# Kernel optimization log

Measured on AMD Instinct MI355X. Metric: run time of the kernel, lower is better.

Reference implementation:

```python
import jax, jax.numpy as jnp
import numpy as np

B, N, D = 32, 50000, 64  # batch, node_num, num_inputs


def setup_inputs() -> dict:
    key = jax.random.key(0)
    k1, k2, k3 = jax.random.split(key, 3)
    x = jax.random.normal(k1, (B, N, D), dtype=jnp.float32)
    # xavier_uniform_ with gain=1.414 on a (2D, 1) matrix: bound = gain*sqrt(6/(fan_in+fan_out))
    bound = 1.414 * np.sqrt(6.0 / (2 * D + 1))
    a = jax.random.uniform(k2, (2 * D, 1), minval=-bound, maxval=bound, dtype=jnp.float32)
    adj_mask = jax.random.randint(k3, (N,), 0, 2).astype(jnp.int32)
    node_index = 123  # scalar target-node index
    return {"x": x, "a": a, "node_index": node_index, "adj_mask": adj_mask}


def reference(x, a, node_index, adj_mask):
    # torch: concat([x[:, idx].expand(node_num), x], -1) @ a  ==  x[:, idx] @ a[:D] + x @ a[D:]
    d = x.shape[-1]
    a_tgt = a[:d, 0]   # weights applied to the (broadcast) target-node features
    a_src = a[d:, 0]   # weights applied to every node's own features
    tgt_score = x[:, node_index] @ a_tgt          # [B]
    e = jax.nn.leaky_relu(tgt_score[:, None] + x @ a_src, negative_slope=0.01)  # [B, N]
    neg = jnp.asarray(-9e15, e.dtype)
    masked = jnp.where(adj_mask > 0, e, neg)
    attention = jax.nn.softmax(masked, axis=1) * adj_mask.astype(e.dtype)[None, :]
    return attention
```

## Files before the change

### kernel.cpp

```cpp
#include <hip/hip_runtime.h>

#define NN 50000
#define DD 64
#define BB 32
#define TILE 256

__global__ __launch_bounds__(256) void attn_pass1(
    const float* __restrict__ x, const float* __restrict__ a,
    const int* __restrict__ node_index, const int* __restrict__ adj,
    float* __restrict__ out, float* __restrict__ sums)
{
    const int tid = threadIdx.x;
    const int b = blockIdx.y;
    const int rowBase = blockIdx.x * TILE;
    const int node = *node_index;

    __shared__ int   sh_adj[TILE];
    __shared__ float sh_p[TILE];
    __shared__ float sh_tgt;
    __shared__ float sh_part[4];

    {
        const int r = rowBase + tid;
        sh_adj[tid] = (r < NN) ? adj[r] : 0;
    }

    if (tid < 64) {
        float v = x[(size_t)b * NN * DD + (size_t)node * DD + tid] * a[tid];
        #pragma unroll
        for (int o = 32; o >= 1; o >>= 1) v += __shfl_xor(v, o, 64);
        if (tid == 0) sh_tgt = v;
    }
    __syncthreads();
    const float tgt = sh_tgt;

    const int wave = tid >> 6;
    const int lane = tid & 63;
    const int g = lane >> 4;
    const int c = lane & 15;

    const float4 av = ((const float4*)(a + DD))[c];
    const float* xb = x + (size_t)b * NN * DD;

    float local = 0.f;

    #pragma unroll
    for (int h = 0; h < 2; h++) {
        int   msk[8];
        float4 xv[8];
        #pragma unroll
        for (int u = 0; u < 8; u++) {
            const int lrow = wave * 64 + h * 32 + u * 4 + g;
            msk[u] = sh_adj[lrow];
            if (msk[u] > 0) {
                const size_t row = (size_t)(rowBase + lrow);
                xv[u] = ((const float4*)(xb + row * DD))[c];
            } else {
                xv[u] = make_float4(0.f, 0.f, 0.f, 0.f);
            }
        }
        #pragma unroll
        for (int u = 0; u < 8; u++) {
            float s = xv[u].x * av.x + xv[u].y * av.y + xv[u].z * av.z + xv[u].w * av.w;
            s += __shfl_xor(s, 1, 64);
            s += __shfl_xor(s, 2, 64);
            s += __shfl_xor(s, 4, 64);
            s += __shfl_xor(s, 8, 64);
            if (c == 0) {
                const int lrow = wave * 64 + h * 32 + u * 4 + g;
                float p = 0.f;
                if (msk[u] > 0) {
                    const float z = tgt + s;
                    const float e = (z > 0.f) ? z : 0.01f * z;
                    p = __expf(e);
                }
                sh_p[lrow] = p;
                local += p;
            }
        }
    }

    #pragma unroll
    for (int o = 32; o >= 1; o >>= 1) local += __shfl_xor(local, o, 64);
    if (lane == 0) sh_part[wave] = local;
    __syncthreads();
    if (tid == 0)
        atomicAdd(&sums[b], sh_part[0] + sh_part[1] + sh_part[2] + sh_part[3]);

    {
        const int r = rowBase + tid;
        if (r < NN) out[(size_t)b * NN + r] = sh_p[tid];
    }
}

__global__ __launch_bounds__(256) void attn_pass2(
    float* __restrict__ out, const float* __restrict__ sums)
{
    const int N4 = NN / 4;
    const int f = blockIdx.x * blockDim.x + threadIdx.x;
    const int b = blockIdx.y;
    if (f < N4) {
        const float inv = 1.0f / sums[b];
        float4* p = (float4*)out + (size_t)b * N4 + f;
        float4 v = *p;
        v.x *= inv; v.y *= inv; v.z *= inv; v.w *= inv;
        *p = v;
    }
}

extern "C" void kernel_launch(void* const* d_in, const int* in_sizes, int n_in,
                              void* d_out, int out_size, void* d_ws, size_t ws_size,
                              hipStream_t stream) {
    const float* x = (const float*)d_in[0];
    const float* a = (const float*)d_in[1];
    const int* node_index = (const int*)d_in[2];
    const int* adj = (const int*)d_in[3];
    float* out = (float*)d_out;
    float* sums = (float*)d_ws;

    hipMemsetAsync(sums, 0, BB * sizeof(float), stream);

    dim3 g1((NN + TILE - 1) / TILE, BB);
    attn_pass1<<<g1, 256, 0, stream>>>(x, a, node_index, adj, out, sums);

    dim3 g2((NN / 4 + 255) / 256, BB);
    attn_pass2<<<g2, 256, 0, stream>>>(out, sums);
}
```

Before: 506.8 us.

## Use 4 lanes per row with strided float4 loads and drop atomics/memset

Pass 1 now assigns 4 lanes per row. Each lane loads four float4 chunks strided across the row, which needs only two shuffle steps instead of four. The per-block partial sums are written to a workspace array instead of being combined with atomicAdd, and pass 2 reduces the 196 partials per batch itself. This removes the memset launch and atomic contention, at the cost of each pass-2 block redundantly re-reducing the partials. The load pattern changes from one contiguous 256B row segment per 16 lanes to interleaved 64B pieces, which could affect coalescing.

```diff
diff --git a/kernel.cpp b/kernel.cpp
--- a/kernel.cpp
+++ b/kernel.cpp
@@ -4,11 +4,12 @@
 #define DD 64
 #define BB 32
 #define TILE 256
+#define NPB ((NN + TILE - 1) / TILE)
 
 __global__ __launch_bounds__(256) void attn_pass1(
     const float* __restrict__ x, const float* __restrict__ a,
     const int* __restrict__ node_index, const int* __restrict__ adj,
-    float* __restrict__ out, float* __restrict__ sums)
+    float* __restrict__ out, float* __restrict__ pbs )
 {
     const int tid = threadIdx.x;
     const int b = blockIdx.y;
@@ -36,47 +37,45 @@
 
     const int wave = tid >> 6;
     const int lane = tid & 63;
-    const int g = lane >> 4;
-    const int c = lane & 15;
+    const int c  = lane & 3;
+    const int rg = lane >> 2;
 
-    const float4 av = ((const float4*)(a + DD))[c];
+    const float4* a4 = (const float4*)(a + DD);
+    const float4 av0 = a4[c + 0];
+    const float4 av1 = a4[c + 4];
+    const float4 av2 = a4[c + 8];
+    const float4 av3 = a4[c + 12];
+
     const float* xb = x + (size_t)b * NN * DD;
-
     float local = 0.f;
 
     #pragma unroll
-    for (int h = 0; h < 2; h++) {
-        int   msk[8];
-        float4 xv[8];
-        #pragma unroll
-        for (int u = 0; u < 8; u++) {
-            const int lrow = wave * 64 + h * 32 + u * 4 + g;
-            msk[u] = sh_adj[lrow];
-            if (msk[u] > 0) {
-                const size_t row = (size_t)(rowBase + lrow);
-                xv[u] = ((const float4*)(xb + row * DD))[c];
-            } else {
-                xv[u] = make_float4(0.f, 0.f, 0.f, 0.f);
+    for (int i = 0; i < 4; i++) {
+        const int lrow = wave * 64 + i * 16 + rg;
+        const int msk = sh_adj[lrow];
+        float s = 0.f;
+        if (msk > 0) {
+            const float4* xr = (const float4*)(xb + (size_t)(rowBase + lrow) * DD);
+            const float4 v0 = xr[c + 0];
+            const float4 v1 = xr[c + 4];
+            const float4 v2 = xr[c + 8];
+            const float4 v3 = xr[c + 12];
+            s  = v0.x * av0.x + v0.y * av0.y + v0.z * av0.z + v0.w * av0.w;
+            s += v1.x * av1.x + v1.y * av1.y + v1.z * av1.z + v1.w * av1.w;
+            s += v2.x * av2.x + v2.y * av2.y + v2.z * av2.z + v2.w * av2.w;
+            s += v3.x * av3.x + v3.y * av3.y + v3.z * av3.z + v3.w * av3.w;
+        }
+        s += __shfl_xor(s, 1, 64);
+        s += __shfl_xor(s, 2, 64);
+        if (c == 0) {
+            float p = 0.f;
+            if (msk > 0) {
+                const float z = tgt + s;
+                const float e = (z > 0.f) ? z : 0.01f * z;
+                p = __expf(e);
             }
-        }
-        #pragma unroll
-        for (int u = 0; u < 8; u++) {
-            float s = xv[u].x * av.x + xv[u].y * av.y + xv[u].z * av.z + xv[u].w * av.w;
-            s += __shfl_xor(s, 1, 64);
-            s += __shfl_xor(s, 2, 64);
-            s += __shfl_xor(s, 4, 64);
-            s += __shfl_xor(s, 8, 64);
-            if (c == 0) {
-                const int lrow = wave * 64 + h * 32 + u * 4 + g;
-                float p = 0.f;
-                if (msk[u] > 0) {
-                    const float z = tgt + s;
-                    const float e = (z > 0.f) ? z : 0.01f * z;
-                    p = __expf(e);
-                }
-                sh_p[lrow] = p;
-                local += p;
-            }
+            sh_p[lrow] = p;
+            local += p;
         }
     }
 
@@ -85,7 +84,7 @@
     if (lane == 0) sh_part[wave] = local;
     __syncthreads();
     if (tid == 0)
-        atomicAdd(&sums[b], sh_part[0] + sh_part[1] + sh_part[2] + sh_part[3]);
+        pbs[b * NPB + blockIdx.x] = sh_part[0] + sh_part[1] + sh_part[2] + sh_part[3];
 
     {
         const int r = rowBase + tid;
@@ -94,17 +93,26 @@
 }
 
 __global__ __launch_bounds__(256) void attn_pass2(
-    float* __restrict__ out, const float* __restrict__ sums)
+    float* __restrict__ out, const float* __restrict__ pbs)
 {
+    const int tid = threadIdx.x;
+    const int b = blockIdx.y;
+    __shared__ float sh[4];
+
+    float v = (tid < NPB) ? pbs[b * NPB + tid] : 0.f;
+    #pragma unroll
+    for (int o = 32; o >= 1; o >>= 1) v += __shfl_xor(v, o, 64);
+    if ((tid & 63) == 0) sh[tid >> 6] = v;
+    __syncthreads();
+    const float inv = 1.0f / (sh[0] + sh[1] + sh[2] + sh[3]);
+
     const int N4 = NN / 4;
-    const int f = blockIdx.x * blockDim.x + threadIdx.x;
-    const int b = blockIdx.y;
+    const int f = blockIdx.x * blockDim.x + tid;
     if (f < N4) {
-        const float inv = 1.0f / sums[b];
         float4* p = (float4*)out + (size_t)b * N4 + f;
-        float4 v = *p;
-        v.x *= inv; v.y *= inv; v.z *= inv; v.w *= inv;
-        *p = v;
+        float4 w = *p;
+        w.x *= inv; w.y *= inv; w.z *= inv; w.w *= inv;
+        *p = w;
     }
 }
 
@@ -116,13 +124,11 @@
     const int* node_index = (const int*)d_in[2];
     const int* adj = (const int*)d_in[3];
     float* out = (float*)d_out;
-    float* sums = (float*)d_ws;
+    float* pbs = (float*)d_ws;
 
-    hipMemsetAsync(sums, 0, BB * sizeof(float), stream);
-
-    dim3 g1((NN + TILE - 1) / TILE, BB);
-    attn_pass1<<<g1, 256, 0, stream>>>(x, a, node_index, adj, out, sums);
+    dim3 g1(NPB, BB);
+    attn_pass1<<<g1, 256, 0, stream>>>(x, a, node_index, adj, out, pbs);
 
     dim3 g2((NN / 4 + 255) / 256, BB);
-    attn_pass2<<<g2, 256, 0, stream>>>(out, sums);
+    attn_pass2<<<g2, 256, 0, stream>>>(out, pbs);
 }
```

Measured after the change: 493.9 us. 1.03x faster.
